# Performance work log

Hardware: AMD Instinct MI355X
Metric: run time of the kernel (lower is better)

Reference implementation:

```python
import jax, jax.numpy as jnp
import numpy as np

B, F_IN, F_OUT, D, K = 32, 64, 64, 512, 64


def setup_inputs() -> dict:
    key = jax.random.key(0)
    k1, k2, k3 = jax.random.split(key, 3)
    x = jax.random.normal(k1, (B, F_IN, D), dtype=jnp.float32)
    # Evaluated monomial-word operators: K matrices of size D x D
    word_ops = jax.random.normal(k2, (K, D, D), dtype=jnp.float32)
    # nn.init.uniform_ -> U[0,1)
    coeff = jax.random.uniform(k3, (F_OUT, F_IN, K), dtype=jnp.float32)
    return {"x": x, "word_ops": word_ops, "coeff": coeff}


def reference(x, word_ops, coeff):
    # Per sample in the torch code:
    #   evals[i, d, k] = (X @ W_k)[i, d] = sum_e X[i, e] * W[k, e, d]
    #   res = tensordot(coeff, evals, ([1, 2], [0, 2]))  -> [F_out, D]
    # Fully batched fused contraction (replaces the Python loop over batch):
    # evals: [B, F_in, D, K]
    evals = jnp.einsum('bie,ked->bidk', x, word_ops)
    # out: [B, F_out, D]
    out = jnp.einsum('oik,bidk->bod', coeff, evals)
    return out
```

## Files before the change

kernel.cpp:

```cpp
#include <hip/hip_runtime.h>


#define KK 32768

typedef __attribute__((ext_vector_type(8))) short bf16x8;
typedef __attribute__((ext_vector_type(4))) float f32x4;

__device__ __forceinline__ unsigned short f2bf(float f) {
  unsigned int u = __float_as_uint(f);
  return (unsigned short)((u + 0x7FFFu + ((u >> 16) & 1u)) >> 16);
}

__device__ __forceinline__ void gld16(void* lds, const void* g) {
  __builtin_amdgcn_global_load_lds((const __attribute__((address_space(1))) void*)g,
                                   (__attribute__((address_space(3))) void*)lds,
                                   16, 0, 0);
}

__global__ __launch_bounds__(256) void convW(const float* __restrict__ W,
                                             unsigned short* __restrict__ WbT) {
  __shared__ float tile[64][65];
  int bx = blockIdx.x;
  int k = bx >> 6, et = (bx >> 3) & 7, dt = bx & 7;
  int t = threadIdx.x;
  const float* src = W + ((size_t)k * 512 + (size_t)et * 64) * 512 + dt * 64;
  int rr = t >> 6, cc = t & 63;
#pragma unroll
  for (int p = 0; p < 16; p++) {
    int e = p * 4 + rr;
    tile[e][cc] = src[(size_t)e * 512 + cc];
  }
  __syncthreads();
  int dl = t >> 4, eg = t & 15;
#pragma unroll
  for (int p = 0; p < 4; p++) {
    int d = p * 16 + dl;
    ushort4 v;
    v.x = f2bf(tile[eg * 4 + 0][d]);
    v.y = f2bf(tile[eg * 4 + 1][d]);
    v.z = f2bf(tile[eg * 4 + 2][d]);
    v.w = f2bf(tile[eg * 4 + 3][d]);
    *(ushort4*)(WbT + (size_t)(dt * 64 + d) * KK + k * 512 + et * 64 + eg * 4) = v;
  }
}

__global__ __launch_bounds__(256) void convX(const float* __restrict__ x,
                                             unsigned short* __restrict__ xT) {
  int tid = blockIdx.x * 256 + threadIdx.x;
  int b = tid >> 15;
  int r = tid & 32767;
  int e = r >> 6, i = r & 63;
  xT[tid] = f2bf(x[((size_t)(b * 64 + i)) * 512 + e]);
}

__global__ __launch_bounds__(256) void convC(const float* __restrict__ c,
                                             unsigned short* __restrict__ cb) {
  int tid = blockIdx.x * 256 + threadIdx.x;
  int k = tid >> 12, r = tid & 4095;
  cb[tid] = f2bf(c[(size_t)r * 64 + k]);
}

__global__ __launch_bounds__(256) void tkern(const unsigned short* __restrict__ xT,
                                             const unsigned short* __restrict__ cb,
                                             unsigned short* __restrict__ Tb) {
  __shared__ unsigned short xe[128 * 88];
  __shared__ unsigned short ck[64 * 64];
  __shared__ unsigned short ot[64 * 136];
  int bx = blockIdx.x;
  int b = bx >> 8, k = (bx >> 2) & 63, eq = bx & 3;
  int t = threadIdx.x;
  {
    const bf16x8* src = (const bf16x8*)(xT + (size_t)b * 32768 + (size_t)eq * 128 * 64);
#pragma unroll
    for (int j = 0; j < 4; j++) {
      int idx = j * 256 + t, e = idx >> 3, c = idx & 7;
      *(bf16x8*)(xe + e * 88 + c * 8) = src[idx];
    }
    const bf16x8* cs = (const bf16x8*)(cb + (size_t)k * 4096);
#pragma unroll
    for (int j = 0; j < 2; j++) *(bf16x8*)(ck + (j * 256 + t) * 8) = cs[j * 256 + t];
  }
  __syncthreads();
  int wid = t >> 6, lane = t & 63, q = lane >> 4, l16 = lane & 15;
  int o0 = wid * 16;
  bf16x8 a0 = *(const bf16x8*)(ck + (o0 + l16) * 64 + q * 8);
  bf16x8 a1 = *(const bf16x8*)(ck + (o0 + l16) * 64 + q * 8 + 32);
#pragma unroll
  for (int et = 0; et < 8; et++) {
    int e = et * 16 + l16;
    bf16x8 b0 = *(const bf16x8*)(xe + e * 88 + q * 8);
    bf16x8 b1 = *(const bf16x8*)(xe + e * 88 + q * 8 + 32);
    f32x4 acc = {0.f, 0.f, 0.f, 0.f};
    acc = __builtin_amdgcn_mfma_f32_16x16x32_bf16(a0, b0, acc, 0, 0, 0);
    acc = __builtin_amdgcn_mfma_f32_16x16x32_bf16(a1, b1, acc, 0, 0, 0);
#pragma unroll
    for (int r2 = 0; r2 < 4; r2++)
      ot[(o0 + q * 4 + r2) * 136 + et * 16 + l16] = f2bf(acc[r2]);
  }
  __syncthreads();
  size_t base = ((size_t)(b * 64)) * KK + k * 512 + eq * 128;
#pragma unroll
  for (int j = 0; j < 4; j++) {
    int idx = j * 256 + t, o = idx >> 4, c = idx & 15;
    *(bf16x8*)(Tb + base + (size_t)o * KK + c * 8) = *(const bf16x8*)(ot + o * 136 + c * 8);
  }
}

__global__ __launch_bounds__(256, 4) void gemm_kern(const unsigned short* __restrict__ A,
                                                    const unsigned short* __restrict__ Bt,
                                                    float* __restrict__ out) {
  __shared__ unsigned short As[128 * 64];
  __shared__ unsigned short Bs[128 * 64];
  int bx = blockIdx.x;
  int ks = bx & 15, nt = (bx >> 4) & 3, mt = bx >> 6;
  int m0 = mt * 128, n0 = nt * 128, k0 = ks * 2048;
  int t = threadIdx.x;
  int wid = t >> 6, lane = t & 63, q = lane >> 4, l16 = lane & 15;
  int wm = (wid & 1) * 64, wn = (wid >> 1) * 64;
  f32x4 acc[4][4] = {};
  int srow = t >> 3;
  int cg = (t & 7) ^ (srow & 7);
  const char* gabase = (const char*)(A + (size_t)m0 * KK + k0) + (size_t)srow * 65536 + cg * 16;
  const char* gbbase = (const char*)(Bt + (size_t)n0 * KK + k0) + (size_t)srow * 65536 + cg * 16;
  int sw0 = q ^ (l16 & 7);
  int sw1 = (4 | q) ^ (l16 & 7);
#pragma unroll 1
  for (int kc = 0; kc < 2048; kc += 64) {
    const char* ga = gabase + (size_t)kc * 2;
    const char* gb = gbbase + (size_t)kc * 2;
#pragma unroll
    for (int j = 0; j < 4; j++) {
      gld16((char*)As + (j * 256 + t) * 16, ga + (size_t)j * 32 * 65536);
      gld16((char*)Bs + (j * 256 + t) * 16, gb + (size_t)j * 32 * 65536);
    }
    __syncthreads();
#pragma unroll
    for (int ks2 = 0; ks2 < 2; ks2++) {
      int slot = ks2 ? sw1 : sw0;
      bf16x8 af[4], bfr[4];
#pragma unroll
      for (int fr = 0; fr < 4; fr++)
        af[fr] = *(const bf16x8*)(As + (wm + fr * 16 + l16) * 64 + slot * 8);
#pragma unroll
      for (int fc = 0; fc < 4; fc++)
        bfr[fc] = *(const bf16x8*)(Bs + (wn + fc * 16 + l16) * 64 + slot * 8);
#pragma unroll
      for (int fr = 0; fr < 4; fr++)
#pragma unroll
        for (int fc = 0; fc < 4; fc++)
          acc[fr][fc] = __builtin_amdgcn_mfma_f32_16x16x32_bf16(af[fr], bfr[fc], acc[fr][fc], 0, 0, 0);
    }
    __syncthreads();
  }
#pragma unroll
  for (int fr = 0; fr < 4; fr++)
#pragma unroll
    for (int fc = 0; fc < 4; fc++)
#pragma unroll
      for (int r = 0; r < 4; r++)
        atomicAdd(&out[(size_t)(m0 + wm + fr * 16 + q * 4 + r) * 512 + n0 + wn + fc * 16 + l16],
                  acc[fr][fc][r]);
}

__global__ __launch_bounds__(256) void fallback_kern(const float* __restrict__ x,
                                                     const float* __restrict__ W,
                                                     const float* __restrict__ coeff,
                                                     float* __restrict__ out) {
  __shared__ float ev[64][129];
  int b = blockIdx.x >> 6, k = blockIdx.x & 63;
  int t = threadIdx.x, dl = t & 127, half = t >> 7;
  const float* xb = x + (size_t)b * 64 * 512;
  const float* Wk = W + (size_t)k * 512 * 512;
  for (int dc = 0; dc < 4; dc++) {
    int d = dc * 128 + dl;
    for (int i = half * 32; i < half * 32 + 32; i++) {
      float acc = 0.f;
      const float* xr = xb + (size_t)i * 512;
#pragma unroll 4
      for (int e = 0; e < 512; e++) acc += xr[e] * Wk[(size_t)e * 512 + d];
      ev[i][dl] = acc;
    }
    __syncthreads();
    for (int o = half * 32; o < half * 32 + 32; o++) {
      float s = 0.f;
#pragma unroll 8
      for (int i = 0; i < 64; i++) s += coeff[((size_t)o * 64 + i) * 64 + k] * ev[i][dl];
      atomicAdd(&out[((size_t)(b * 64 + o)) * 512 + d], s);
    }
    __syncthreads();
  }
}

extern "C" void kernel_launch(void* const* d_in, const int* in_sizes, int n_in,
                              void* d_out, int out_size, void* d_ws, size_t ws_size,
                              hipStream_t stream) {
  const float* x = (const float*)d_in[0];
  const float* W = (const float*)d_in[1];
  const float* coeff = (const float*)d_in[2];
  float* out = (float*)d_out;
  const size_t OFF_XT = 33554432;
  const size_t OFF_CB = OFF_XT + 2097152;
  const size_t OFF_TB = OFF_CB + 524288;
  const size_t NEED = OFF_TB + 134217728;

  hipMemsetAsync(d_out, 0, (size_t)out_size * sizeof(float), stream);
  if (ws_size >= NEED) {
    unsigned short* WbT = (unsigned short*)d_ws;
    unsigned short* xT  = (unsigned short*)((char*)d_ws + OFF_XT);
    unsigned short* cb  = (unsigned short*)((char*)d_ws + OFF_CB);
    unsigned short* Tb  = (unsigned short*)((char*)d_ws + OFF_TB);
    convW<<<4096, 256, 0, stream>>>(W, WbT);
    convX<<<4096, 256, 0, stream>>>(x, xT);
    convC<<<1024, 256, 0, stream>>>(coeff, cb);
    tkern<<<8192, 256, 0, stream>>>(xT, cb, Tb);
    gemm_kern<<<1024, 256, 0, stream>>>(Tb, WbT, out);
  } else {
    fallback_kern<<<2048, 256, 0, stream>>>(x, W, coeff, out);
  }
}
```

Measured before the change: 251.9 us.

## Restructure T-kernel to loop over k with double-buffered coeff tiles; tile transposes

The precompute kernel now handles four k values per block. Coefficient tiles are double-buffered in LDS and loaded with async global-to-LDS loads into XOR-swizzled layouts, while the x tile is loaded once and reused across all four k. The convX and convC transposes now go through an LDS tile, so global reads and writes are both coalesced instead of strided. This cuts block count and redundant x loads in exchange for more registers per block and a longer per-block serial loop.

```diff
diff --git a/kernel.cpp b/kernel.cpp
--- a/kernel.cpp
+++ b/kernel.cpp
@@ -46,63 +46,134 @@
 
 __global__ __launch_bounds__(256) void convX(const float* __restrict__ x,
                                              unsigned short* __restrict__ xT) {
-  int tid = blockIdx.x * 256 + threadIdx.x;
-  int b = tid >> 15;
-  int r = tid & 32767;
-  int e = r >> 6, i = r & 63;
-  xT[tid] = f2bf(x[((size_t)(b * 64 + i)) * 512 + e]);
+  __shared__ unsigned short lds[64 * 130];
+  int bx = blockIdx.x;
+  int b = bx >> 2, ec = bx & 3;
+  int t = threadIdx.x;
+  const float* src = x + (size_t)b * 32768 + ec * 128;
+#pragma unroll
+  for (int j = 0; j < 32; j++) {
+    int idx = j * 256 + t;
+    int i = idx >> 7, e = idx & 127;
+    lds[i * 130 + e] = f2bf(src[(size_t)i * 512 + e]);
+  }
+  __syncthreads();
+  unsigned short* dst = xT + (size_t)b * 32768 + ec * 128 * 64;
+#pragma unroll
+  for (int j = 0; j < 32; j++) {
+    int idx = j * 256 + t;
+    int e = idx >> 6, i = idx & 63;
+    dst[idx] = lds[i * 130 + e];
+  }
 }
 
 __global__ __launch_bounds__(256) void convC(const float* __restrict__ c,
                                              unsigned short* __restrict__ cb) {
-  int tid = blockIdx.x * 256 + threadIdx.x;
-  int k = tid >> 12, r = tid & 4095;
-  cb[tid] = f2bf(c[(size_t)r * 64 + k]);
-}
-
-__global__ __launch_bounds__(256) void tkern(const unsigned short* __restrict__ xT,
-                                             const unsigned short* __restrict__ cb,
-                                             unsigned short* __restrict__ Tb) {
-  __shared__ unsigned short xe[128 * 88];
-  __shared__ unsigned short ck[64 * 64];
-  __shared__ unsigned short ot[64 * 136];
-  int bx = blockIdx.x;
-  int b = bx >> 8, k = (bx >> 2) & 63, eq = bx & 3;
+  __shared__ unsigned short lds[64 * 66];
+  int rb = blockIdx.x;
+  int t = threadIdx.x;
+  const float* src = c + (size_t)rb * 4096;
+#pragma unroll
+  for (int j = 0; j < 16; j++) {
+    int idx = j * 256 + t;
+    int r = idx >> 6, k = idx & 63;
+    lds[r * 66 + k] = f2bf(src[idx]);
+  }
+  __syncthreads();
+#pragma unroll
+  for (int j = 0; j < 16; j++) {
+    int idx = j * 256 + t;
+    int k = idx >> 6, r = idx & 63;
+    cb[(size_t)k * 4096 + rb * 64 + r] = lds[r * 66 + k];
+  }
+}
+
+__global__ __launch_bounds__(256, 2) void tkern(const unsigned short* __restrict__ xT,
+                                                const unsigned short* __restrict__ cb,
+                                                unsigned short* __restrict__ Tb) {
+  __shared__ unsigned short xe[128 * 64];
+  __shared__ unsigned short ckb[2][64 * 64];
+  __shared__ unsigned short ot[64 * 132];
+  int bx = blockIdx.x;
+  int eq = bx & 3, kq = (bx >> 2) & 15, b = bx >> 6;
   int t = threadIdx.x;
   {
-    const bf16x8* src = (const bf16x8*)(xT + (size_t)b * 32768 + (size_t)eq * 128 * 64);
+    const unsigned short* gx = xT + (size_t)b * 32768 + (size_t)eq * 8192;
 #pragma unroll
     for (int j = 0; j < 4; j++) {
-      int idx = j * 256 + t, e = idx >> 3, c = idx & 7;
-      *(bf16x8*)(xe + e * 88 + c * 8) = src[idx];
-    }
-    const bf16x8* cs = (const bf16x8*)(cb + (size_t)k * 4096);
-#pragma unroll
-    for (int j = 0; j < 2; j++) *(bf16x8*)(ck + (j * 256 + t) * 8) = cs[j * 256 + t];
-  }
-  __syncthreads();
+      int idx = j * 256 + t;
+      int e = idx >> 3, cg = (idx & 7) ^ (e & 7);
+      gld16((char*)xe + idx * 16, gx + e * 64 + cg * 8);
+    }
+    const unsigned short* gc = cb + (size_t)(kq * 4) * 4096;
+#pragma unroll
+    for (int j = 0; j < 2; j++) {
+      int idx = j * 256 + t;
+      int o = idx >> 3, cg = (idx & 7) ^ (o & 7);
+      gld16((char*)ckb[0] + idx * 16, gc + o * 64 + cg * 8);
+    }
+  }
   int wid = t >> 6, lane = t & 63, q = lane >> 4, l16 = lane & 15;
-  int o0 = wid * 16;
-  bf16x8 a0 = *(const bf16x8*)(ck + (o0 + l16) * 64 + q * 8);
-  bf16x8 a1 = *(const bf16x8*)(ck + (o0 + l16) * 64 + q * 8 + 32);
-#pragma unroll
-  for (int et = 0; et < 8; et++) {
-    int e = et * 16 + l16;
-    bf16x8 b0 = *(const bf16x8*)(xe + e * 88 + q * 8);
-    bf16x8 b1 = *(const bf16x8*)(xe + e * 88 + q * 8 + 32);
-    f32x4 acc = {0.f, 0.f, 0.f, 0.f};
-    acc = __builtin_amdgcn_mfma_f32_16x16x32_bf16(a0, b0, acc, 0, 0, 0);
-    acc = __builtin_amdgcn_mfma_f32_16x16x32_bf16(a1, b1, acc, 0, 0, 0);
-#pragma unroll
-    for (int r2 = 0; r2 < 4; r2++)
-      ot[(o0 + q * 4 + r2) * 136 + et * 16 + l16] = f2bf(acc[r2]);
-  }
-  __syncthreads();
-  size_t base = ((size_t)(b * 64)) * KK + k * 512 + eq * 128;
-#pragma unroll
-  for (int j = 0; j < 4; j++) {
-    int idx = j * 256 + t, o = idx >> 4, c = idx & 15;
-    *(bf16x8*)(Tb + base + (size_t)o * KK + c * 8) = *(const bf16x8*)(ot + o * 136 + c * 8);
+  size_t mbase = (size_t)(b * 64) * KK;
+#pragma unroll 1
+  for (int kj = 0; kj < 4; kj++) {
+    int cur = kj & 1;
+    __syncthreads();
+    if (kj < 3) {
+      const unsigned short* gc = cb + (size_t)(kq * 4 + kj + 1) * 4096;
+#pragma unroll
+      for (int j = 0; j < 2; j++) {
+        int idx = j * 256 + t;
+        int o = idx >> 3, cg = (idx & 7) ^ (o & 7);
+        gld16((char*)ckb[cur ^ 1] + idx * 16, gc + o * 64 + cg * 8);
+      }
+    }
+    const unsigned short* ck = ckb[cur];
+    f32x4 acc[4][2] = {};
+    bf16x8 af[4][2], bfr[2][2];
+#pragma unroll
+    for (int mf = 0; mf < 4; mf++)
+#pragma unroll
+      for (int ks2 = 0; ks2 < 2; ks2++) {
+        int row = mf * 16 + l16;
+        int s2 = (ks2 * 4 + q) ^ (row & 7);
+        af[mf][ks2] = *(const bf16x8*)(ck + row * 64 + s2 * 8);
+      }
+#pragma unroll
+    for (int nf = 0; nf < 2; nf++) {
+      int e = wid * 32 + nf * 16 + l16;
+#pragma unroll
+      for (int ks2 = 0; ks2 < 2; ks2++) {
+        int s2 = (ks2 * 4 + q) ^ (e & 7);
+        bfr[nf][ks2] = *(const bf16x8*)(xe + e * 64 + s2 * 8);
+      }
+    }
+#pragma unroll
+    for (int mf = 0; mf < 4; mf++)
+#pragma unroll
+      for (int nf = 0; nf < 2; nf++)
+#pragma unroll
+        for (int ks2 = 0; ks2 < 2; ks2++)
+          acc[mf][nf] = __builtin_amdgcn_mfma_f32_16x16x32_bf16(af[mf][ks2], bfr[nf][ks2],
+                                                                acc[mf][nf], 0, 0, 0);
+#pragma unroll
+    for (int mf = 0; mf < 4; mf++)
+#pragma unroll
+      for (int nf = 0; nf < 2; nf++)
+#pragma unroll
+        for (int r = 0; r < 4; r++) {
+          int o = mf * 16 + q * 4 + r;
+          int e = wid * 32 + nf * 16 + l16;
+          ot[o * 132 + e] = f2bf(acc[mf][nf][r]);
+        }
+    __syncthreads();
+    unsigned short* gdst = Tb + mbase + (size_t)(kq * 4 + kj) * 512 + eq * 128;
+#pragma unroll
+    for (int j = 0; j < 8; j++) {
+      int idx = j * 256 + t;
+      int o = idx >> 5, c = idx & 31;
+      *(ushort4*)(gdst + (size_t)o * KK + c * 4) = *(const ushort4*)(ot + o * 132 + c * 4);
+    }
   }
 }
 
@@ -209,10 +280,10 @@
     unsigned short* xT  = (unsigned short*)((char*)d_ws + OFF_XT);
     unsigned short* cb  = (unsigned short*)((char*)d_ws + OFF_CB);
     unsigned short* Tb  = (unsigned short*)((char*)d_ws + OFF_TB);
+    convX<<<128, 256, 0, stream>>>(x, xT);
+    convC<<<64, 256, 0, stream>>>(coeff, cb);
     convW<<<4096, 256, 0, stream>>>(W, WbT);
-    convX<<<4096, 256, 0, stream>>>(x, xT);
-    convC<<<1024, 256, 0, stream>>>(coeff, cb);
-    tkern<<<8192, 256, 0, stream>>>(xT, cb, Tb);
+    tkern<<<2048, 256, 0, stream>>>(xT, cb, Tb);
     gemm_kern<<<1024, 256, 0, stream>>>(Tb, WbT, out);
   } else {
     fallback_kern<<<2048, 256, 0, stream>>>(x, W, coeff, out);
```

Result: faster. 246.9 us (-2.0%).
